# Optimization experiments

Measured on AMD Instinct MI355X. Metric: run time of the kernel, lower is better.

Reference implementation:

```python
import jax, jax.numpy as jnp
import numpy as np

HIDDEN = 1024
FFN = 4096
NUM_EXPERTS = 8
LB_WEIGHT = 0.01
BATCH, SEQ = 4, 1024


def setup_inputs() -> dict:
    key = jax.random.key(0)
    ks = jax.random.split(key, 6)
    s_h = 1.0 / np.sqrt(HIDDEN)
    s_f = 1.0 / np.sqrt(FFN)
    return {
        "x": jax.random.normal(ks[0], (BATCH, SEQ, HIDDEN), dtype=jnp.float32),
        "router_w": jax.random.uniform(ks[1], (NUM_EXPERTS, HIDDEN), jnp.float32, -s_h, s_h),
        "fc1_w": jax.random.uniform(ks[2], (NUM_EXPERTS, FFN, HIDDEN), jnp.float32, -s_h, s_h),
        "fc1_b": jax.random.uniform(ks[3], (NUM_EXPERTS, FFN), jnp.float32, -s_h, s_h),
        "fc2_w": jax.random.uniform(ks[4], (NUM_EXPERTS, HIDDEN, FFN), jnp.float32, -s_f, s_f),
        "fc2_b": jax.random.uniform(ks[5], (NUM_EXPERTS, HIDDEN), jnp.float32, -s_f, s_f),
    }


def reference(x, router_w, fc1_w, fc1_b, fc2_w, fc2_b):
    B, S, H = x.shape
    E = router_w.shape[0]
    T = B * S
    xf = x.reshape(T, H)

    # Router: top-1 over softmax probs
    logits = xf @ router_w.T                     # [T, E]
    probs = jax.nn.softmax(logits, axis=-1)      # [T, E]
    expert_weights = jnp.max(probs, axis=-1)     # [T]
    expert_idx = jnp.argmax(probs, axis=-1)      # [T] int

    # Expert MLPs computed densely for all experts (faithful math; jit-friendly
    # replacement for the dynamic-shaped per-expert gather/scatter).
    h = jax.nn.gelu(jnp.einsum('td,efd->etf', xf, fc1_w) + fc1_b[:, None, :],
                    approximate=False)                      # [E, T, F]
    out_all = jnp.einsum('etf,ehf->eth', h, fc2_w) + fc2_b[:, None, :]  # [E, T, H]

    # Select each token's assigned expert output, scaled by its gate weight.
    out_flat = out_all[expert_idx, jnp.arange(T)] * expert_weights[:, None]  # [T, H]
    output = out_flat.reshape(B, S, H)

    # Load balance loss
    mean_probs = probs.mean(axis=0)                                   # [E]
    counts = jnp.bincount(expert_idx, length=E).astype(jnp.float32)   # [E]
    freq = counts / T
    aux_loss = LB_WEIGHT * E * jnp.sum(mean_probs * freq)
    return output, aux_loss
```

## Files before the change

kernel.cpp:

```cpp
#include <hip/hip_runtime.h>
#include <cstdint>

#define HID 1024
#define FFN 4096
#define NE 8
#define NT 4096

typedef __bf16 bf16x8 __attribute__((ext_vector_type(8)));
typedef unsigned short ushortx8 __attribute__((ext_vector_type(8)));
typedef float f32x4 __attribute__((ext_vector_type(4)));


__device__ __forceinline__ unsigned pk_bf16(float a, float b) {
  unsigned ua = __float_as_uint(a), ub = __float_as_uint(b);
  ua = (ua + 0x7fffu + ((ua >> 16) & 1u)) >> 16;
  ub = (ub + 0x7fffu + ((ub >> 16) & 1u)) >> 16;
  return ua | (ub << 16);
}
__device__ __forceinline__ unsigned short f2bf(float a) {
  unsigned ua = __float_as_uint(a);
  return (unsigned short)((ua + 0x7fffu + ((ua >> 16) & 1u)) >> 16);
}

__global__ __launch_bounds__(256) void router_kernel(
    const float* __restrict__ x, const float* __restrict__ rw,
    int* __restrict__ counts, float* __restrict__ prob_sum,
    int* __restrict__ eidx, float* __restrict__ wgt) {
  __shared__ float rsm[NE * HID];
  __shared__ float pshare[4][NE];
  for (int i = threadIdx.x; i < NE * HID; i += 256) rsm[i] = rw[i];
  __syncthreads();
  int wave = threadIdx.x >> 6, lane = threadIdx.x & 63;
  int t = blockIdx.x * 4 + wave;
  const float* xr = x + (size_t)t * HID;
  float acc[NE];
#pragma unroll
  for (int e = 0; e < NE; e++) acc[e] = 0.f;
#pragma unroll
  for (int j = 0; j < HID / 64; j++) {
    float xv = xr[j * 64 + lane];
#pragma unroll
    for (int e = 0; e < NE; e++) acc[e] = fmaf(xv, rsm[e * HID + j * 64 + lane], acc[e]);
  }
#pragma unroll
  for (int off = 32; off > 0; off >>= 1) {
#pragma unroll
    for (int e = 0; e < NE; e++) acc[e] += __shfl_down(acc[e], off);
  }
  if (lane == 0) {
    float mx = acc[0]; int mi = 0;
#pragma unroll
    for (int e = 1; e < NE; e++) if (acc[e] > mx) { mx = acc[e]; mi = e; }
    float pr[NE], se = 0.f;
#pragma unroll
    for (int e = 0; e < NE; e++) { pr[e] = expf(acc[e] - mx); se += pr[e]; }
    float inv = 1.f / se;
    wgt[t] = pr[mi] * inv;
    eidx[t] = mi;
    atomicAdd(&counts[mi], 1);
#pragma unroll
    for (int e = 0; e < NE; e++) pshare[wave][e] = pr[e] * inv;
  }
  __syncthreads();
  if (threadIdx.x < NE) {
    float s = pshare[0][threadIdx.x] + pshare[1][threadIdx.x] +
              pshare[2][threadIdx.x] + pshare[3][threadIdx.x];
    atomicAdd(&prob_sum[threadIdx.x], s);
  }
}

__global__ void scan_aux_kernel(const int* __restrict__ counts,
                                const float* __restrict__ prob_sum,
                                int* __restrict__ offsets,
                                float* __restrict__ aux_out) {
  if (threadIdx.x == 0) {
    int off = 0; float s = 0.f;
    for (int e = 0; e < NE; e++) {
      offsets[e] = off;
      off += counts[e];
      s += (prob_sum[e] / (float)NT) * ((float)counts[e] / (float)NT);
    }
    *aux_out = 0.01f * (float)NE * s;
  }
}

__global__ void bucketize_kernel(const int* __restrict__ eidx,
                                 const int* __restrict__ offsets,
                                 int* __restrict__ cursor, int* __restrict__ perm) {
  int t = blockIdx.x * 256 + threadIdx.x;
  int e = eidx[t];
  int slot = atomicAdd(&cursor[e], 1);
  perm[offsets[e] + slot] = t;
}

__global__ __launch_bounds__(256) void gemm1_kernel(
    const float* __restrict__ x, const float* __restrict__ w1,
    const float* __restrict__ b1, const int* __restrict__ counts,
    const int* __restrict__ offsets, const int* __restrict__ perm,
    unsigned short* __restrict__ hbuf) {
  int e = blockIdx.z;
  int Nexp = counts[e];
  int m0 = blockIdx.y * 128;
  if (m0 >= Nexp) return;
  int n0 = blockIdx.x * 128;
  int obase = offsets[e];
  int gbase = obase + m0;

  __shared__ unsigned short As[128 * 40];
  __shared__ unsigned short Bs[128 * 40];
  __shared__ int toks[128];

  int tid = threadIdx.x;
  if (tid < 128) {
    int r = m0 + tid;
    toks[tid] = perm[obase + (r < Nexp ? r : Nexp - 1)];
  }
  __syncthreads();

  int tr = tid >> 3;
  int tc = tid & 7;
  const float* w1e = w1 + (size_t)e * FFN * HID;
  const float* aptr[4];
  const float* bptr[4];
#pragma unroll
  for (int i = 0; i < 4; i++) {
    aptr[i] = x + (size_t)toks[tr + 32 * i] * HID + tc * 4;
    bptr[i] = w1e + (size_t)(n0 + tr + 32 * i) * HID + tc * 4;
  }

  int lane = tid & 63, w = tid >> 6;
  int wm = w & 1, wn = w >> 1;
  int quad = lane >> 4, l15 = lane & 15;
  f32x4 acc[4][4] = {};
  const int std_idx = tr * 40 + tc * 4;

  for (int kk = 0; kk < HID / 32; kk++) {
#pragma unroll
    for (int i = 0; i < 4; i++) {
      float4 av = *(const float4*)(aptr[i] + kk * 32);
      float4 bv = *(const float4*)(bptr[i] + kk * 32);
      uint2 ap; ap.x = pk_bf16(av.x, av.y); ap.y = pk_bf16(av.z, av.w);
      uint2 bp; bp.x = pk_bf16(bv.x, bv.y); bp.y = pk_bf16(bv.z, bv.w);
      *(uint2*)&As[std_idx + i * 32 * 40] = ap;
      *(uint2*)&Bs[std_idx + i * 32 * 40] = bp;
    }
    __syncthreads();
    bf16x8 af[4], bfr[4];
#pragma unroll
    for (int mt = 0; mt < 4; mt++) {
      ushortx8 raw = *(const ushortx8*)&As[(wm * 64 + mt * 16 + l15) * 40 + quad * 8];
      af[mt] = __builtin_bit_cast(bf16x8, raw);
    }
#pragma unroll
    for (int nt = 0; nt < 4; nt++) {
      ushortx8 raw = *(const ushortx8*)&Bs[(wn * 64 + nt * 16 + l15) * 40 + quad * 8];
      bfr[nt] = __builtin_bit_cast(bf16x8, raw);
    }
#pragma unroll
    for (int mt = 0; mt < 4; mt++)
#pragma unroll
      for (int nt = 0; nt < 4; nt++)
        acc[mt][nt] = __builtin_amdgcn_mfma_f32_16x16x32_bf16(af[mt], bfr[nt], acc[mt][nt], 0, 0, 0);
    __syncthreads();
  }

  int mrem = Nexp - m0;
#pragma unroll
  for (int mt = 0; mt < 4; mt++) {
    int rbase = wm * 64 + mt * 16 + quad * 4;
#pragma unroll
    for (int nt = 0; nt < 4; nt++) {
      int col = wn * 64 + nt * 16 + l15;
      float bb = b1[e * FFN + n0 + col];
#pragma unroll
      for (int r = 0; r < 4; r++) {
        int rr = rbase + r;
        if (rr < mrem) {
          float v = acc[mt][nt][r] + bb;
          v = 0.5f * v * (1.0f + erff(v * 0.70710678118654752f));
          hbuf[(size_t)(gbase + rr) * FFN + n0 + col] = f2bf(v);
        }
      }
    }
  }
}

__global__ __launch_bounds__(256) void gemm2_kernel(
    const unsigned short* __restrict__ hbuf, const float* __restrict__ w2,
    const float* __restrict__ b2, const int* __restrict__ counts,
    const int* __restrict__ offsets, const int* __restrict__ perm,
    const float* __restrict__ wgt, float* __restrict__ out) {
  int e = blockIdx.z;
  int Nexp = counts[e];
  int m0 = blockIdx.y * 128;
  if (m0 >= Nexp) return;
  int n0 = blockIdx.x * 128;
  int obase = offsets[e];
  int gbase = obase + m0;

  __shared__ unsigned short As[128 * 40];
  __shared__ unsigned short Bs[128 * 40];
  __shared__ int toks[128];
  __shared__ float wsh[128];

  int tid = threadIdx.x;
  if (tid < 128) {
    int r = m0 + tid;
    int tk = perm[obase + (r < Nexp ? r : Nexp - 1)];
    toks[tid] = tk;
    wsh[tid] = wgt[tk];
  }
  __syncthreads();

  int tr2 = tid >> 2, tc2 = tid & 3;
  int g0 = gbase + tr2;     if (g0 > NT - 1) g0 = NT - 1;
  int g1 = gbase + tr2 + 64; if (g1 > NT - 1) g1 = NT - 1;
  const unsigned short* ap0 = hbuf + (size_t)g0 * FFN + tc2 * 8;
  const unsigned short* ap1 = hbuf + (size_t)g1 * FFN + tc2 * 8;

  int tr = tid >> 3, tc = tid & 7;
  const float* w2e = w2 + (size_t)e * HID * FFN;
  const float* bptr[4];
#pragma unroll
  for (int i = 0; i < 4; i++)
    bptr[i] = w2e + (size_t)(n0 + tr + 32 * i) * FFN + tc * 4;

  int lane = tid & 63, w = tid >> 6;
  int wm = w & 1, wn = w >> 1;
  int quad = lane >> 4, l15 = lane & 15;
  f32x4 acc[4][4] = {};

  for (int kk = 0; kk < FFN / 32; kk++) {
    uint4 a0 = *(const uint4*)(ap0 + kk * 32);
    uint4 a1 = *(const uint4*)(ap1 + kk * 32);
    float4 bv[4];
#pragma unroll
    for (int i = 0; i < 4; i++) bv[i] = *(const float4*)(bptr[i] + kk * 32);
    *(uint4*)&As[tr2 * 40 + tc2 * 8] = a0;
    *(uint4*)&As[(tr2 + 64) * 40 + tc2 * 8] = a1;
#pragma unroll
    for (int i = 0; i < 4; i++) {
      uint2 bp; bp.x = pk_bf16(bv[i].x, bv[i].y); bp.y = pk_bf16(bv[i].z, bv[i].w);
      *(uint2*)&Bs[(tr + 32 * i) * 40 + tc * 4] = bp;
    }
    __syncthreads();
    bf16x8 af[4], bfr[4];
#pragma unroll
    for (int mt = 0; mt < 4; mt++) {
      ushortx8 raw = *(const ushortx8*)&As[(wm * 64 + mt * 16 + l15) * 40 + quad * 8];
      af[mt] = __builtin_bit_cast(bf16x8, raw);
    }
#pragma unroll
    for (int nt = 0; nt < 4; nt++) {
      ushortx8 raw = *(const ushortx8*)&Bs[(wn * 64 + nt * 16 + l15) * 40 + quad * 8];
      bfr[nt] = __builtin_bit_cast(bf16x8, raw);
    }
#pragma unroll
    for (int mt = 0; mt < 4; mt++)
#pragma unroll
      for (int nt = 0; nt < 4; nt++)
        acc[mt][nt] = __builtin_amdgcn_mfma_f32_16x16x32_bf16(af[mt], bfr[nt], acc[mt][nt], 0, 0, 0);
    __syncthreads();
  }

  int mrem = Nexp - m0;
#pragma unroll
  for (int mt = 0; mt < 4; mt++) {
    int rbase = wm * 64 + mt * 16 + quad * 4;
#pragma unroll
    for (int nt = 0; nt < 4; nt++) {
      int col = wn * 64 + nt * 16 + l15;
      float bb = b2[e * HID + n0 + col];
#pragma unroll
      for (int r = 0; r < 4; r++) {
        int rr = rbase + r;
        if (rr < mrem) {
          float v = (acc[mt][nt][r] + bb) * wsh[rr];
          out[(size_t)toks[rr] * HID + n0 + col] = v;
        }
      }
    }
  }
}

extern "C" void kernel_launch(void* const* d_in, const int* in_sizes, int n_in,
                              void* d_out, int out_size, void* d_ws, size_t ws_size,
                              hipStream_t stream) {
  const float* x  = (const float*)d_in[0];
  const float* rw = (const float*)d_in[1];
  const float* w1 = (const float*)d_in[2];
  const float* b1 = (const float*)d_in[3];
  const float* w2 = (const float*)d_in[4];
  const float* b2 = (const float*)d_in[5];
  float* out = (float*)d_out;

  char* ws = (char*)d_ws;
  int*   counts   = (int*)(ws + 0);
  int*   cursor   = (int*)(ws + 32);
  float* prob_sum = (float*)(ws + 64);
  int*   offsets  = (int*)(ws + 96);
  int*   perm     = (int*)(ws + 256);
  float* wgt      = (float*)(ws + 256 + 16384);
  int*   eidx     = (int*)(ws + 256 + 32768);
  unsigned short* hbuf = (unsigned short*)(ws + 65536);

  hipMemsetAsync(d_ws, 0, 128, stream);
  router_kernel<<<NT / 4, 256, 0, stream>>>(x, rw, counts, prob_sum, eidx, wgt);
  scan_aux_kernel<<<1, 64, 0, stream>>>(counts, prob_sum, offsets, out + (size_t)NT * HID);
  bucketize_kernel<<<NT / 256, 256, 0, stream>>>(eidx, offsets, cursor, perm);
  gemm1_kernel<<<dim3(FFN / 128, NT / 128, NE), 256, 0, stream>>>(x, w1, b1, counts, offsets, perm, hbuf);
  gemm2_kernel<<<dim3(HID / 128, NT / 128, NE), 256, 0, stream>>>(hbuf, w2, b2, counts, offsets, perm, wgt, out);
}
```

Measured before the change: 625.0 us.

## Pre-convert weights to bf16, gather tokens, async LDS loads, split-K gemm2

Adds a pass that converts both expert weight tensors to bf16 on every call, and a gather kernel that packs routed tokens into contiguous bf16 rows. Both GEMMs now load tiles with global_load_lds into swizzled, double-buffered LDS and declare launch bounds for four blocks per CU. gemm2 splits K four ways and accumulates into a zeroed output with atomics. The intent is to remove per-tile fp32-to-bf16 conversion and gathered loads from the GEMM loops and to raise gemm2 parallelism. In exchange, every call pays extra full passes over the weights plus an output memset and atomic traffic.

```diff
diff --git a/kernel.cpp b/kernel.cpp
--- a/kernel.cpp
+++ b/kernel.cpp
@@ -5,13 +5,14 @@
 #define FFN 4096
 #define NE 8
 #define NT 4096
+#define NTP 4224
 
 typedef __bf16 bf16x8 __attribute__((ext_vector_type(8)));
 typedef unsigned short ushortx8 __attribute__((ext_vector_type(8)));
 typedef float f32x4 __attribute__((ext_vector_type(4)));
 
 
-__device__ __forceinline__ unsigned pk_bf16(float a, float b) {
+__device__ __forceinline__ unsigned cvt2(float a, float b) {
   unsigned ua = __float_as_uint(a), ub = __float_as_uint(b);
   ua = (ua + 0x7fffu + ((ua >> 16) & 1u)) >> 16;
   ub = (ub + 0x7fffu + ((ub >> 16) & 1u)) >> 16;
@@ -20,6 +21,29 @@
 __device__ __forceinline__ unsigned short f2bf(float a) {
   unsigned ua = __float_as_uint(a);
   return (unsigned short)((ua + 0x7fffu + ((ua >> 16) & 1u)) >> 16);
+}
+__device__ __forceinline__ void ldg16(const unsigned short* g, unsigned short* l) {
+  __builtin_amdgcn_global_load_lds((const __attribute__((address_space(1))) void*)g,
+                                   (__attribute__((address_space(3))) void*)l, 16, 0, 0);
+}
+
+__global__ __launch_bounds__(256) void wcvt_kernel(const float* __restrict__ w1,
+                                                   const float* __restrict__ w2,
+                                                   unsigned short* __restrict__ w1b,
+                                                   unsigned short* __restrict__ w2b) {
+  size_t t = (size_t)blockIdx.x * 256 + threadIdx.x;
+  const size_t half = (size_t)NE * FFN * HID / 8;
+  const float* src;
+  unsigned short* dst;
+  size_t i;
+  if (t < half) { src = w1; dst = w1b; i = t; }
+  else          { src = w2; dst = w2b; i = t - half; }
+  float4 v0 = *(const float4*)(src + i * 8);
+  float4 v1 = *(const float4*)(src + i * 8 + 4);
+  uint4 o;
+  o.x = cvt2(v0.x, v0.y); o.y = cvt2(v0.z, v0.w);
+  o.z = cvt2(v1.x, v1.y); o.w = cvt2(v1.z, v1.w);
+  *(uint4*)(dst + i * 8) = o;
 }
 
 __global__ __launch_bounds__(256) void router_kernel(
@@ -93,69 +117,71 @@
   perm[offsets[e] + slot] = t;
 }
 
-__global__ __launch_bounds__(256) void gemm1_kernel(
-    const float* __restrict__ x, const float* __restrict__ w1,
+__global__ __launch_bounds__(256) void xgather_kernel(
+    const float* __restrict__ x, const int* __restrict__ perm,
+    const float* __restrict__ wgt, unsigned short* __restrict__ xg,
+    float* __restrict__ wgtg) {
+  int row = blockIdx.x;
+  int tok = perm[row];
+  float4 v = ((const float4*)(x + (size_t)tok * HID))[threadIdx.x];
+  uint2 o; o.x = cvt2(v.x, v.y); o.y = cvt2(v.z, v.w);
+  ((uint2*)(xg + (size_t)row * HID))[threadIdx.x] = o;
+  if (threadIdx.x == 0) wgtg[row] = wgt[tok];
+}
+
+
+__global__ __launch_bounds__(256, 4) void gemm1_kernel(
+    const unsigned short* __restrict__ xg, const unsigned short* __restrict__ w1b,
     const float* __restrict__ b1, const int* __restrict__ counts,
-    const int* __restrict__ offsets, const int* __restrict__ perm,
-    unsigned short* __restrict__ hbuf) {
+    const int* __restrict__ offsets, unsigned short* __restrict__ hbuf) {
   int e = blockIdx.z;
   int Nexp = counts[e];
   int m0 = blockIdx.y * 128;
   if (m0 >= Nexp) return;
   int n0 = blockIdx.x * 128;
-  int obase = offsets[e];
-  int gbase = obase + m0;
-
-  __shared__ unsigned short As[128 * 40];
-  __shared__ unsigned short Bs[128 * 40];
-  __shared__ int toks[128];
-
-  int tid = threadIdx.x;
-  if (tid < 128) {
-    int r = m0 + tid;
-    toks[tid] = perm[obase + (r < Nexp ? r : Nexp - 1)];
-  }
+  int gbase = offsets[e] + m0;
+
+  __shared__ unsigned short As[2][128 * 32];
+  __shared__ unsigned short Bs[2][128 * 32];
+
+  int tid = threadIdx.x, lane = tid & 63, w = tid >> 6;
+  int rl = lane >> 2, kbp = lane & 3;
+  int rA0 = w * 32 + rl, rA1 = rA0 + 16;
+  int s0 = (rA0 + (rA0 >> 2)) & 3, s1 = (rA1 + (rA1 >> 2)) & 3;
+  const unsigned short* w1e = w1b + (size_t)e * (FFN * HID);
+  const unsigned short* ga0 = xg + (size_t)(gbase + rA0) * HID + (kbp ^ s0) * 8;
+  const unsigned short* ga1 = xg + (size_t)(gbase + rA1) * HID + (kbp ^ s1) * 8;
+  const unsigned short* gb0 = w1e + (size_t)(n0 + rA0) * HID + (kbp ^ s0) * 8;
+  const unsigned short* gb1 = w1e + (size_t)(n0 + rA1) * HID + (kbp ^ s1) * 8;
+  const int ld0 = (w * 32) * 32, ld1 = (w * 32 + 16) * 32;
+
+  int wm = w & 1, wn = w >> 1, quad = lane >> 4, l15 = lane & 15;
+  int sl = (l15 + (l15 >> 2)) & 3;
+  const int aoff = (wm * 64 + l15) * 32 + (quad ^ sl) * 8;
+  const int boff = (wn * 64 + l15) * 32 + (quad ^ sl) * 8;
+  f32x4 acc[4][4] = {};
+
+  ldg16(ga0, &As[0][ld0]); ldg16(ga1, &As[0][ld1]);
+  ldg16(gb0, &Bs[0][ld0]); ldg16(gb1, &Bs[0][ld1]);
+  ga0 += 32; ga1 += 32; gb0 += 32; gb1 += 32;
   __syncthreads();
 
-  int tr = tid >> 3;
-  int tc = tid & 7;
-  const float* w1e = w1 + (size_t)e * FFN * HID;
-  const float* aptr[4];
-  const float* bptr[4];
-#pragma unroll
-  for (int i = 0; i < 4; i++) {
-    aptr[i] = x + (size_t)toks[tr + 32 * i] * HID + tc * 4;
-    bptr[i] = w1e + (size_t)(n0 + tr + 32 * i) * HID + tc * 4;
-  }
-
-  int lane = tid & 63, w = tid >> 6;
-  int wm = w & 1, wn = w >> 1;
-  int quad = lane >> 4, l15 = lane & 15;
-  f32x4 acc[4][4] = {};
-  const int std_idx = tr * 40 + tc * 4;
-
-  for (int kk = 0; kk < HID / 32; kk++) {
-#pragma unroll
-    for (int i = 0; i < 4; i++) {
-      float4 av = *(const float4*)(aptr[i] + kk * 32);
-      float4 bv = *(const float4*)(bptr[i] + kk * 32);
-      uint2 ap; ap.x = pk_bf16(av.x, av.y); ap.y = pk_bf16(av.z, av.w);
-      uint2 bp; bp.x = pk_bf16(bv.x, bv.y); bp.y = pk_bf16(bv.z, bv.w);
-      *(uint2*)&As[std_idx + i * 32 * 40] = ap;
-      *(uint2*)&Bs[std_idx + i * 32 * 40] = bp;
-    }
-    __syncthreads();
+  const int NK = HID / 32;
+  for (int kk = 0; kk < NK; kk++) {
+    int cur = kk & 1;
+    if (kk + 1 < NK) {
+      int nb = cur ^ 1;
+      ldg16(ga0, &As[nb][ld0]); ldg16(ga1, &As[nb][ld1]);
+      ldg16(gb0, &Bs[nb][ld0]); ldg16(gb1, &Bs[nb][ld1]);
+      ga0 += 32; ga1 += 32; gb0 += 32; gb1 += 32;
+    }
     bf16x8 af[4], bfr[4];
 #pragma unroll
-    for (int mt = 0; mt < 4; mt++) {
-      ushortx8 raw = *(const ushortx8*)&As[(wm * 64 + mt * 16 + l15) * 40 + quad * 8];
-      af[mt] = __builtin_bit_cast(bf16x8, raw);
-    }
-#pragma unroll
-    for (int nt = 0; nt < 4; nt++) {
-      ushortx8 raw = *(const ushortx8*)&Bs[(wn * 64 + nt * 16 + l15) * 40 + quad * 8];
-      bfr[nt] = __builtin_bit_cast(bf16x8, raw);
-    }
+    for (int mt = 0; mt < 4; mt++)
+      af[mt] = __builtin_bit_cast(bf16x8, *(const ushortx8*)&As[cur][aoff + mt * 512]);
+#pragma unroll
+    for (int nt = 0; nt < 4; nt++)
+      bfr[nt] = __builtin_bit_cast(bf16x8, *(const ushortx8*)&Bs[cur][boff + nt * 512]);
 #pragma unroll
     for (int mt = 0; mt < 4; mt++)
 #pragma unroll
@@ -185,76 +211,60 @@
   }
 }
 
-__global__ __launch_bounds__(256) void gemm2_kernel(
-    const unsigned short* __restrict__ hbuf, const float* __restrict__ w2,
+__global__ __launch_bounds__(256, 4) void gemm2_kernel(
+    const unsigned short* __restrict__ hbuf, const unsigned short* __restrict__ w2b,
     const float* __restrict__ b2, const int* __restrict__ counts,
     const int* __restrict__ offsets, const int* __restrict__ perm,
-    const float* __restrict__ wgt, float* __restrict__ out) {
-  int e = blockIdx.z;
+    const float* __restrict__ wgtg, float* __restrict__ out) {
+  int e = blockIdx.z & 7, kz = blockIdx.z >> 3;
   int Nexp = counts[e];
   int m0 = blockIdx.y * 128;
   if (m0 >= Nexp) return;
   int n0 = blockIdx.x * 128;
-  int obase = offsets[e];
-  int gbase = obase + m0;
-
-  __shared__ unsigned short As[128 * 40];
-  __shared__ unsigned short Bs[128 * 40];
-  __shared__ int toks[128];
-  __shared__ float wsh[128];
-
-  int tid = threadIdx.x;
-  if (tid < 128) {
-    int r = m0 + tid;
-    int tk = perm[obase + (r < Nexp ? r : Nexp - 1)];
-    toks[tid] = tk;
-    wsh[tid] = wgt[tk];
-  }
+  int k0 = kz * (FFN / 4);
+  int gbase = offsets[e] + m0;
+
+  __shared__ unsigned short As[2][128 * 32];
+  __shared__ unsigned short Bs[2][128 * 32];
+
+  int tid = threadIdx.x, lane = tid & 63, w = tid >> 6;
+  int rl = lane >> 2, kbp = lane & 3;
+  int rA0 = w * 32 + rl, rA1 = rA0 + 16;
+  int s0 = (rA0 + (rA0 >> 2)) & 3, s1 = (rA1 + (rA1 >> 2)) & 3;
+  const unsigned short* w2e = w2b + (size_t)e * (HID * FFN);
+  const unsigned short* ga0 = hbuf + (size_t)(gbase + rA0) * FFN + k0 + (kbp ^ s0) * 8;
+  const unsigned short* ga1 = hbuf + (size_t)(gbase + rA1) * FFN + k0 + (kbp ^ s1) * 8;
+  const unsigned short* gb0 = w2e + (size_t)(n0 + rA0) * FFN + k0 + (kbp ^ s0) * 8;
+  const unsigned short* gb1 = w2e + (size_t)(n0 + rA1) * FFN + k0 + (kbp ^ s1) * 8;
+  const int ld0 = (w * 32) * 32, ld1 = (w * 32 + 16) * 32;
+
+  int wm = w & 1, wn = w >> 1, quad = lane >> 4, l15 = lane & 15;
+  int sl = (l15 + (l15 >> 2)) & 3;
+  const int aoff = (wm * 64 + l15) * 32 + (quad ^ sl) * 8;
+  const int boff = (wn * 64 + l15) * 32 + (quad ^ sl) * 8;
+  f32x4 acc[4][4] = {};
+
+  ldg16(ga0, &As[0][ld0]); ldg16(ga1, &As[0][ld1]);
+  ldg16(gb0, &Bs[0][ld0]); ldg16(gb1, &Bs[0][ld1]);
+  ga0 += 32; ga1 += 32; gb0 += 32; gb1 += 32;
   __syncthreads();
 
-  int tr2 = tid >> 2, tc2 = tid & 3;
-  int g0 = gbase + tr2;     if (g0 > NT - 1) g0 = NT - 1;
-  int g1 = gbase + tr2 + 64; if (g1 > NT - 1) g1 = NT - 1;
-  const unsigned short* ap0 = hbuf + (size_t)g0 * FFN + tc2 * 8;
-  const unsigned short* ap1 = hbuf + (size_t)g1 * FFN + tc2 * 8;
-
-  int tr = tid >> 3, tc = tid & 7;
-  const float* w2e = w2 + (size_t)e * HID * FFN;
-  const float* bptr[4];
-#pragma unroll
-  for (int i = 0; i < 4; i++)
-    bptr[i] = w2e + (size_t)(n0 + tr + 32 * i) * FFN + tc * 4;
-
-  int lane = tid & 63, w = tid >> 6;
-  int wm = w & 1, wn = w >> 1;
-  int quad = lane >> 4, l15 = lane & 15;
-  f32x4 acc[4][4] = {};
-
-  for (int kk = 0; kk < FFN / 32; kk++) {
-    uint4 a0 = *(const uint4*)(ap0 + kk * 32);
-    uint4 a1 = *(const uint4*)(ap1 + kk * 32);
-    float4 bv[4];
-#pragma unroll
-    for (int i = 0; i < 4; i++) bv[i] = *(const float4*)(bptr[i] + kk * 32);
-    *(uint4*)&As[tr2 * 40 + tc2 * 8] = a0;
-    *(uint4*)&As[(tr2 + 64) * 40 + tc2 * 8] = a1;
-#pragma unroll
-    for (int i = 0; i < 4; i++) {
-      uint2 bp; bp.x = pk_bf16(bv[i].x, bv[i].y); bp.y = pk_bf16(bv[i].z, bv[i].w);
-      *(uint2*)&Bs[(tr + 32 * i) * 40 + tc * 4] = bp;
-    }
-    __syncthreads();
+  const int NK = (FFN / 4) / 32;
+  for (int kk = 0; kk < NK; kk++) {
+    int cur = kk & 1;
+    if (kk + 1 < NK) {
+      int nb = cur ^ 1;
+      ldg16(ga0, &As[nb][ld0]); ldg16(ga1, &As[nb][ld1]);
+      ldg16(gb0, &Bs[nb][ld0]); ldg16(gb1, &Bs[nb][ld1]);
+      ga0 += 32; ga1 += 32; gb0 += 32; gb1 += 32;
+    }
     bf16x8 af[4], bfr[4];
 #pragma unroll
-    for (int mt = 0; mt < 4; mt++) {
-      ushortx8 raw = *(const ushortx8*)&As[(wm * 64 + mt * 16 + l15) * 40 + quad * 8];
-      af[mt] = __builtin_bit_cast(bf16x8, raw);
-    }
-#pragma unroll
-    for (int nt = 0; nt < 4; nt++) {
-      ushortx8 raw = *(const ushortx8*)&Bs[(wn * 64 + nt * 16 + l15) * 40 + quad * 8];
-      bfr[nt] = __builtin_bit_cast(bf16x8, raw);
-    }
+    for (int mt = 0; mt < 4; mt++)
+      af[mt] = __builtin_bit_cast(bf16x8, *(const ushortx8*)&As[cur][aoff + mt * 512]);
+#pragma unroll
+    for (int nt = 0; nt < 4; nt++)
+      bfr[nt] = __builtin_bit_cast(bf16x8, *(const ushortx8*)&Bs[cur][boff + nt * 512]);
 #pragma unroll
     for (int mt = 0; mt < 4; mt++)
 #pragma unroll
@@ -267,6 +277,12 @@
 #pragma unroll
   for (int mt = 0; mt < 4; mt++) {
     int rbase = wm * 64 + mt * 16 + quad * 4;
+    int tk[4]; float gt[4];
+#pragma unroll
+    for (int r = 0; r < 4; r++) {
+      int ri = gbase + rbase + r; if (ri > NT - 1) ri = NT - 1;
+      tk[r] = perm[ri]; gt[r] = wgtg[ri];
+    }
 #pragma unroll
     for (int nt = 0; nt < 4; nt++) {
       int col = wn * 64 + nt * 16 + l15;
@@ -275,8 +291,9 @@
       for (int r = 0; r < 4; r++) {
         int rr = rbase + r;
         if (rr < mrem) {
-          float v = (acc[mt][nt][r] + bb) * wsh[rr];
-          out[(size_t)toks[rr] * HID + n0 + col] = v;
+          float v = acc[mt][nt][r];
+          if (kz == 0) v += bb;
+          atomicAdd(out + (size_t)tk[r] * HID + n0 + col, v * gt[r]);
         }
       }
     }
@@ -300,14 +317,21 @@
   float* prob_sum = (float*)(ws + 64);
   int*   offsets  = (int*)(ws + 96);
   int*   perm     = (int*)(ws + 256);
-  float* wgt      = (float*)(ws + 256 + 16384);
-  int*   eidx     = (int*)(ws + 256 + 32768);
-  unsigned short* hbuf = (unsigned short*)(ws + 65536);
-
-  hipMemsetAsync(d_ws, 0, 128, stream);
+  float* wgt      = (float*)(ws + 16640);
+  int*   eidx     = (int*)(ws + 33024);
+  float* wgtg     = (float*)(ws + 49408);
+  unsigned short* xg   = (unsigned short*)(ws + 65792);
+  unsigned short* w1b  = (unsigned short*)(ws + 8716544);
+  unsigned short* hbuf = (unsigned short*)(ws + 75825408);
+  unsigned short* w2b  = (unsigned short*)(ws + 110428416);
+
+  (void)hipMemsetAsync(d_ws, 0, 128, stream);
+  (void)hipMemsetAsync(d_out, 0, (size_t)(NT * HID + 1) * sizeof(float), stream);
+  wcvt_kernel<<<32768, 256, 0, stream>>>(w1, w2, w1b, w2b);
   router_kernel<<<NT / 4, 256, 0, stream>>>(x, rw, counts, prob_sum, eidx, wgt);
   scan_aux_kernel<<<1, 64, 0, stream>>>(counts, prob_sum, offsets, out + (size_t)NT * HID);
   bucketize_kernel<<<NT / 256, 256, 0, stream>>>(eidx, offsets, cursor, perm);
-  gemm1_kernel<<<dim3(FFN / 128, NT / 128, NE), 256, 0, stream>>>(x, w1, b1, counts, offsets, perm, hbuf);
-  gemm2_kernel<<<dim3(HID / 128, NT / 128, NE), 256, 0, stream>>>(hbuf, w2, b2, counts, offsets, perm, wgt, out);
-}
+  xgather_kernel<<<NT, 256, 0, stream>>>(x, perm, wgt, xg, wgtg);
+  gemm1_kernel<<<dim3(FFN / 128, NT / 128, NE), 256, 0, stream>>>(xg, w1b, b1, counts, offsets, hbuf);
+  gemm2_kernel<<<dim3(HID / 128, NT / 128, NE * 4), 256, 0, stream>>>(hbuf, w2b, b2, counts, offsets, perm, wgtg, out);
+}
```

After: 600.4 us. 1.04x faster.
